# Kernel tuning notes

Measured on AMD Instinct MI355X. Metric: run time of the kernel, lower is better.

Reference implementation:

```python
import jax, jax.numpy as jnp
import numpy as np

SIG_DEPTH = 4  # matches sig_depth init arg


def _outer(a, b):
    # flattened tensor product: [B, m] x [B, n] -> [B, m*n] (row-major, matches signatory layout)
    return (a[:, :, None] * b[:, None, :]).reshape(a.shape[0], -1)


def setup_inputs() -> dict:
    key = jax.random.key(0)
    k1, k2 = jax.random.split(key)
    B, L, Cin = 64, 256, 7
    out_dim = 512
    C = Cin + 1
    sig_channels = sum(C ** k for k in range(1, SIG_DEPTH + 1))  # 4680
    inp = jax.random.normal(k1, (B, L, Cin), dtype=jnp.float32)
    W = jax.random.normal(k2, (out_dim, sig_channels), dtype=jnp.float32) * 0.02
    b = jnp.zeros((out_dim,), dtype=jnp.float32)
    return {"inp": inp, "W": W, "b": b}


def reference(inp, W, b):
    B, L, Cin = inp.shape
    # Augment: prepend time channel linspace(0, 1, L), keep original channels
    t = jnp.broadcast_to(jnp.linspace(0.0, 1.0, L, dtype=inp.dtype)[None, :, None], (B, L, 1))
    x = jnp.concatenate([t, inp], axis=-1)  # [B, L, C]
    C = Cin + 1
    d = SIG_DEPTH
    dx = jnp.transpose(x[:, 1:] - x[:, :-1], (1, 0, 2))  # [L-1, B, C] increments
    init = tuple(jnp.zeros((B, C ** (k + 1)), x.dtype) for k in range(d))  # identity signature (all zero levels)

    def step(levels, v):
        # exp(v) in the truncated tensor algebra: e_k = v^{(x)k} / k!
        e = [v]
        for k in range(1, d):
            e.append(_outer(e[-1], v) / (k + 1))
        # Chen's identity: new_k = a_k + e_k + sum_{i=1}^{k-1} a_i (x) e_{k-i}
        new = []
        for k in range(d):
            acc = levels[k] + e[k]
            for i in range(k):
                acc = acc + _outer(levels[i], e[k - 1 - i])
            new.append(acc)
        sig = jnp.concatenate(new, axis=-1)  # [B, sig_channels]
        return tuple(new), sig

    _, sigs = jax.lax.scan(step, init, dx)  # [L-1, B, sig_channels] (stream=True)
    sigs = jnp.transpose(sigs, (1, 0, 2))   # [B, L-1, sig_channels]
    return sigs @ W.T + b                   # [B, L-1, out_dim]
```

## Files before the change

### kernel.cpp

```cpp
#include <hip/hip_runtime.h>
#include <hip/hip_bf16.h>

#define BATCH 64
#define LSEQ 256
#define CIN 7
#define CC 8
#define NSIG 4680
#define KPAD 4736
#define TSTEPS 255
#define ODIM 512
#define NCHUNK 16
#define CH 16
#define NKT 74
#define BM 256
#define BN 128

typedef __attribute__((ext_vector_type(8))) unsigned short ushort8;
typedef __attribute__((ext_vector_type(8))) __bf16 bf16x8;
typedef __attribute__((ext_vector_type(4))) float f32x4;

__device__ __forceinline__ unsigned short f2bf(float x) {
    __hip_bfloat16 h = __float2bfloat16(x);
    return *(unsigned short*)&h;
}

#define GLDS16(gp, lp)                                                      \
    __builtin_amdgcn_global_load_lds(                                       \
        (const __attribute__((address_space(1))) void*)(gp),                \
        (__attribute__((address_space(3))) void*)(lp), 16, 0, 0)

__global__ __launch_bounds__(512) void sig_ckpt_kernel(const float* __restrict__ inp,
                                                       float* __restrict__ ckpt) {
    __shared__ float sDx[TSTEPS * CC];

    const int b   = blockIdx.x;
    const int tid = threadIdx.x;

    const float* ip = inp + (size_t)b * LSEQ * CIN;
    for (int i = tid; i < TSTEPS * CC; i += 512) {
        int t = i >> 3, c = i & 7;
        sDx[i] = (c == 0) ? (1.0f / 255.0f)
                          : ip[(t + 1) * CIN + (c - 1)] - ip[t * CIN + (c - 1)];
    }
    __syncthreads();

    const int i1 = tid >> 6;
    const int i2 = (tid >> 3) & 7;
    const int i3 = tid & 7;

    float a1own = 0.0f, a2own = 0.0f, a3 = 0.0f;
    float a4[8];
#pragma unroll
    for (int e = 0; e < 8; ++e) a4[e] = 0.0f;

    for (int t = 0; t < 240; ++t) {
        const float* v = &sDx[t * CC];
        const float4 vlo = *(const float4*)&v[0];
        const float4 vhi = *(const float4*)&v[4];
        const float va = v[i1], vb = v[i2], vc = v[i3];
        const float e3s = va * vb * vc * (1.0f / 6.0f);
        const float T4 = e3s * 0.25f + a1own * vb * vc * (1.0f / 6.0f)
                       + a2own * vc * 0.5f + a3;
        a4[0] += vlo.x * T4; a4[1] += vlo.y * T4;
        a4[2] += vlo.z * T4; a4[3] += vlo.w * T4;
        a4[4] += vhi.x * T4; a4[5] += vhi.y * T4;
        a4[6] += vhi.z * T4; a4[7] += vhi.w * T4;
        a3 += e3s + (a1own * vb * 0.5f + a2own) * vc;
        a2own += vb * (0.5f * va + a1own);
        a1own += va;

        if (((t + 1) & 15) == 0) {
            const int c = ((t + 1) >> 4) - 1;
            float* cp = ckpt + ((size_t)b * 15 + c) * NSIG;
            if ((tid & 63) == 0) cp[i1] = a1own;
            if ((tid & 7) == 0) cp[8 + (tid >> 3)] = a2own;
            cp[72 + tid] = a3;
            float4 q0 = {a4[0], a4[1], a4[2], a4[3]};
            float4 q1 = {a4[4], a4[5], a4[6], a4[7]};
            *(float4*)&cp[584 + tid * 8]     = q0;
            *(float4*)&cp[584 + tid * 8 + 4] = q1;
        }
    }
}

__global__ __launch_bounds__(512) void sig_write_kernel(const float* __restrict__ inp,
                                                        const float* __restrict__ ckpt,
                                                        unsigned short* __restrict__ sig) {
    __shared__ float sDx[CH * CC];

    const int chunk = blockIdx.x;
    const int b     = blockIdx.y;
    const int tid   = threadIdx.x;
    const int t0    = chunk * CH;
    const int t1    = (chunk == NCHUNK - 1) ? TSTEPS : t0 + CH;

    const float* ip = inp + (size_t)b * LSEQ * CIN;
    for (int i = tid; i < (t1 - t0) * CC; i += 512) {
        int t = t0 + (i >> 3), c = i & 7;
        sDx[i] = (c == 0) ? (1.0f / 255.0f)
                          : ip[(t + 1) * CIN + (c - 1)] - ip[t * CIN + (c - 1)];
    }
    __syncthreads();

    const int i1 = tid >> 6;
    const int i2 = (tid >> 3) & 7;
    const int i3 = tid & 7;

    float a1own, a2own, a3;
    float a4[8];
    if (chunk == 0) {
        a1own = a2own = a3 = 0.0f;
#pragma unroll
        for (int e = 0; e < 8; ++e) a4[e] = 0.0f;
    } else {
        const float* cp = ckpt + ((size_t)b * 15 + (chunk - 1)) * NSIG;
        a1own = cp[i1];
        a2own = cp[8 + (tid >> 3)];
        a3    = cp[72 + tid];
        float4 q0 = *(const float4*)&cp[584 + tid * 8];
        float4 q1 = *(const float4*)&cp[584 + tid * 8 + 4];
        a4[0] = q0.x; a4[1] = q0.y; a4[2] = q0.z; a4[3] = q0.w;
        a4[4] = q1.x; a4[5] = q1.y; a4[6] = q1.z; a4[7] = q1.w;
    }

    for (int t = t0; t < t1; ++t) {
        const float* v = &sDx[(t - t0) * CC];
        const float4 vlo = *(const float4*)&v[0];
        const float4 vhi = *(const float4*)&v[4];
        const float va = v[i1], vb = v[i2], vc = v[i3];
        const float e3s = va * vb * vc * (1.0f / 6.0f);
        const float T4 = e3s * 0.25f + a1own * vb * vc * (1.0f / 6.0f)
                       + a2own * vc * 0.5f + a3;
        a4[0] += vlo.x * T4; a4[1] += vlo.y * T4;
        a4[2] += vlo.z * T4; a4[3] += vlo.w * T4;
        a4[4] += vhi.x * T4; a4[5] += vhi.y * T4;
        a4[6] += vhi.z * T4; a4[7] += vhi.w * T4;
        a3 += e3s + (a1own * vb * 0.5f + a2own) * vc;
        a2own += vb * (0.5f * va + a1own);
        a1own += va;

        unsigned short* row = sig + ((size_t)b * TSTEPS + t) * KPAD;
        ushort8 pack;
#pragma unroll
        for (int e = 0; e < 8; ++e) pack[e] = f2bf(a4[e]);
        *(ushort8*)(row + 584 + tid * 8) = pack;
        row[72 + tid] = f2bf(a3);
        if ((tid & 63) == 0) row[i1] = f2bf(a1own);
        if ((tid & 7) == 0) row[8 + (tid >> 3)] = f2bf(a2own);
        if (tid >= 448 && tid < 504) row[4232 + tid] = 0;
    }
}

__global__ __launch_bounds__(256) void wcvt_kernel(const float* __restrict__ W,
                                                   unsigned short* __restrict__ Wb) {
    int idx = blockIdx.x * 256 + threadIdx.x;
    if (idx >= ODIM * KPAD) return;
    int n = idx / KPAD, k = idx - n * KPAD;
    Wb[idx] = (k < NSIG) ? f2bf(W[(size_t)n * NSIG + k]) : (unsigned short)0;
}

__global__ __launch_bounds__(512) void gemm_kernel(const unsigned short* __restrict__ A,
                                                   const unsigned short* __restrict__ Wb,
                                                   const float* __restrict__ bias,
                                                   float* __restrict__ out,
                                                   int Mrows) {
    __shared__ unsigned short As[3][BM * 64];
    __shared__ unsigned short Bs[3][BN * 64];

    const int tid = threadIdx.x;
    int nt, mt;
    if (gridDim.y == 64) {
        const int li = blockIdx.y * 4 + blockIdx.x;
        const int x  = li & 7;
        const int j  = li >> 3;
        mt = x * 8 + (j >> 2);
        nt = j & 3;
    } else {
        nt = blockIdx.x; mt = blockIdx.y;
    }
    const int lane = tid & 63;
    const int wv   = tid >> 6;
    const int wr   = wv >> 1;
    const int wc   = wv & 1;
    const int lr   = lane & 15;
    const int lq   = lane >> 4;
    const int sb   = lr & 7;

    const f32x4 z4 = {0.0f, 0.0f, 0.0f, 0.0f};
    f32x4 acc[4][4];
#pragma unroll
    for (int i = 0; i < 4; ++i)
#pragma unroll
        for (int j = 0; j < 4; ++j) acc[i][j] = z4;

    const int srow = tid >> 3;
    const int gcb  = (tid & 7) ^ (srow & 7);
    const int scol = gcb * 8;

    const unsigned short* aptr[4];
    const unsigned short* bptr[2];
#pragma unroll
    for (int i = 0; i < 4; ++i) {
        int gr = mt * BM + i * 64 + srow;
        if (gr >= Mrows) gr = 0;
        aptr[i] = A + (size_t)gr * KPAD + scol;
    }
#pragma unroll
    for (int i = 0; i < 2; ++i)
        bptr[i] = Wb + (size_t)(nt * BN + i * 64 + srow) * KPAD + scol;

    const int kel0 = ((lq)     ^ sb) * 8;
    const int kel1 = ((4 + lq) ^ sb) * 8;

    const int aoff = (wr * 64 + lr) * 64;
    const int boff = (wc * 64 + lr) * 64;

#define STAGE_ALL(buf, koff)                                                \
    do {                                                                    \
        _Pragma("unroll")                                                   \
        for (int i_ = 0; i_ < 4; ++i_)                                      \
            GLDS16(aptr[i_] + (koff),                                       \
                   ((char*)As[buf]) + i_ * 8192 + tid * 16);                \
        _Pragma("unroll")                                                   \
        for (int i_ = 0; i_ < 2; ++i_)                                      \
            GLDS16(bptr[i_] + (koff),                                       \
                   ((char*)Bs[buf]) + i_ * 8192 + tid * 16);                \
    } while (0)

    STAGE_ALL(0, 0);
    STAGE_ALL(1, 64);
    asm volatile("s_waitcnt vmcnt(6)" ::: "memory");
    __builtin_amdgcn_sched_barrier(0);
    __builtin_amdgcn_s_barrier();
    __builtin_amdgcn_sched_barrier(0);

    bf16x8 afP[4], bfP[4], afN[4], bfN[4];
    {
        const unsigned short* as0 = &As[0][0];
        const unsigned short* bs0 = &Bs[0][0];
#pragma unroll
        for (int i = 0; i < 4; ++i)
            afP[i] = *(const bf16x8*)&as0[aoff + i * 1024 + kel0];
#pragma unroll
        for (int j = 0; j < 4; ++j)
            bfP[j] = *(const bf16x8*)&bs0[boff + j * 1024 + kel0];
    }
    __builtin_amdgcn_sched_barrier(0);

    int cur = 0, nxt = 1, nn = 2;
    for (int t = 0; t < NKT; ++t) {
        const unsigned short* as = &As[0][0] + cur * (BM * 64);
        const unsigned short* bs = &Bs[0][0] + cur * (BN * 64);

#pragma unroll
        for (int i = 0; i < 4; ++i)
            afN[i] = *(const bf16x8*)&as[aoff + i * 1024 + kel1];
#pragma unroll
        for (int j = 0; j < 4; ++j)
            bfN[j] = *(const bf16x8*)&bs[boff + j * 1024 + kel1];
        if (t + 2 < NKT) STAGE_ALL(nn, (t + 2) * 64);
        __builtin_amdgcn_sched_barrier(0);

        asm volatile("s_waitcnt lgkmcnt(8)" ::: "memory");
        __builtin_amdgcn_sched_barrier(0);
        __builtin_amdgcn_s_setprio(1);
#pragma unroll
        for (int i = 0; i < 4; ++i)
#pragma unroll
            for (int j = 0; j < 4; ++j)
                acc[i][j] = __builtin_amdgcn_mfma_f32_16x16x32_bf16(
                    afP[i], bfP[j], acc[i][j], 0, 0, 0);
        __builtin_amdgcn_s_setprio(0);
        __builtin_amdgcn_sched_barrier(0);

        asm volatile("s_waitcnt lgkmcnt(0)" ::: "memory");
        __builtin_amdgcn_sched_barrier(0);
        if (t + 1 < NKT) {
            if (t + 2 < NKT) {
                asm volatile("s_waitcnt vmcnt(6)" ::: "memory");
            } else {
                asm volatile("s_waitcnt vmcnt(0)" ::: "memory");
            }
            __builtin_amdgcn_sched_barrier(0);
            __builtin_amdgcn_s_barrier();
            __builtin_amdgcn_sched_barrier(0);
            const unsigned short* asn = &As[0][0] + nxt * (BM * 64);
            const unsigned short* bsn = &Bs[0][0] + nxt * (BN * 64);
#pragma unroll
            for (int i = 0; i < 4; ++i)
                afP[i] = *(const bf16x8*)&asn[aoff + i * 1024 + kel0];
#pragma unroll
            for (int j = 0; j < 4; ++j)
                bfP[j] = *(const bf16x8*)&bsn[boff + j * 1024 + kel0];
            __builtin_amdgcn_sched_barrier(0);
        }

        __builtin_amdgcn_s_setprio(1);
#pragma unroll
        for (int i = 0; i < 4; ++i)
#pragma unroll
            for (int j = 0; j < 4; ++j)
                acc[i][j] = __builtin_amdgcn_mfma_f32_16x16x32_bf16(
                    afN[i], bfN[j], acc[i][j], 0, 0, 0);
        __builtin_amdgcn_s_setprio(0);
        __builtin_amdgcn_sched_barrier(0);

        const int tmp = cur; cur = nxt; nxt = nn; nn = tmp;
    }

    float bn[4];
#pragma unroll
    for (int j = 0; j < 4; ++j)
        bn[j] = bias[nt * BN + wc * 64 + j * 16 + lr];

#pragma unroll
    for (int i = 0; i < 4; ++i) {
        const int mbase = mt * BM + wr * 64 + i * 16 + lq * 4;
#pragma unroll
        for (int r = 0; r < 4; ++r) {
            const int m = mbase + r;
            if (m < Mrows) {
#pragma unroll
                for (int j = 0; j < 4; ++j) {
                    const int n = nt * BN + wc * 64 + j * 16 + lr;
                    out[(size_t)m * ODIM + n] = acc[i][j][r] + bn[j];
                }
            }
        }
    }
#undef STAGE_ALL
}

extern "C" void kernel_launch(void* const* d_in, const int* in_sizes, int n_in,
                              void* d_out, int out_size, void* d_ws, size_t ws_size,
                              hipStream_t stream) {
    const float* inp  = (const float*)d_in[0];
    const float* W    = (const float*)d_in[1];
    const float* bias = (const float*)d_in[2];
    float* out = (float*)d_out;

    const size_t wbBytes = (size_t)ODIM * KPAD * sizeof(unsigned short);
    const size_t sigPB   = (size_t)TSTEPS * KPAD * sizeof(unsigned short);
    const size_t ckptPB  = (size_t)15 * NSIG * sizeof(float);
    const size_t perB    = sigPB + ckptPB;

    int nbMax = (int)((ws_size - wbBytes) / perB);
    if (nbMax > BATCH) nbMax = BATCH;
    if (nbMax < 1) nbMax = 1;

    unsigned short* sig  = (unsigned short*)d_ws;
    float*          ckpt = (float*)((char*)d_ws + (size_t)nbMax * sigPB);
    unsigned short* Wb   = (unsigned short*)((char*)d_ws + (ws_size - wbBytes));

    wcvt_kernel<<<(ODIM * KPAD + 255) / 256, 256, 0, stream>>>(W, Wb);

    for (int b0 = 0; b0 < BATCH; b0 += nbMax) {
        const int nb = (b0 + nbMax <= BATCH) ? nbMax : (BATCH - b0);
        const int Mrows = nb * TSTEPS;
        const float* ipb = inp + (size_t)b0 * LSEQ * CIN;
        sig_ckpt_kernel<<<nb, 512, 0, stream>>>(ipb, ckpt);
        sig_write_kernel<<<dim3(NCHUNK, nb), 512, 0, stream>>>(ipb, ckpt, sig);
        gemm_kernel<<<dim3(ODIM / BN, (Mrows + BM - 1) / BM), 512, 0, stream>>>(
            sig, Wb, bias, out + (size_t)b0 * TSTEPS * ODIM, Mrows);
    }
}
```

Measured before the change: 148.5 us.

## Fuse weight conversion into checkpoint kernel and split checkpoint work per batch

```diff
diff --git a/kernel.cpp b/kernel.cpp
--- a/kernel.cpp
+++ b/kernel.cpp
@@ -14,6 +14,7 @@
 #define NKT 74
 #define BM 256
 #define BN 128
+#define WCVT_BLK 592
 
 typedef __attribute__((ext_vector_type(8))) unsigned short ushort8;
 typedef __attribute__((ext_vector_type(8))) __bf16 bf16x8;
@@ -29,56 +30,74 @@
         (const __attribute__((address_space(1))) void*)(gp),                \
         (__attribute__((address_space(3))) void*)(lp), 16, 0, 0)
 
-__global__ __launch_bounds__(512) void sig_ckpt_kernel(const float* __restrict__ inp,
-                                                       float* __restrict__ ckpt) {
+__global__ __launch_bounds__(512) void prep_kernel(const float* __restrict__ inp,
+                                                   float* __restrict__ ckpt,
+                                                   const float* __restrict__ W,
+                                                   unsigned short* __restrict__ Wb,
+                                                   int nb) {
     __shared__ float sDx[TSTEPS * CC];
-
-    const int b   = blockIdx.x;
+    const int bx  = blockIdx.x;
     const int tid = threadIdx.x;
 
-    const float* ip = inp + (size_t)b * LSEQ * CIN;
-    for (int i = tid; i < TSTEPS * CC; i += 512) {
-        int t = i >> 3, c = i & 7;
-        sDx[i] = (c == 0) ? (1.0f / 255.0f)
-                          : ip[(t + 1) * CIN + (c - 1)] - ip[t * CIN + (c - 1)];
-    }
-    __syncthreads();
-
-    const int i1 = tid >> 6;
-    const int i2 = (tid >> 3) & 7;
-    const int i3 = tid & 7;
-
-    float a1own = 0.0f, a2own = 0.0f, a3 = 0.0f;
-    float a4[8];
-#pragma unroll
-    for (int e = 0; e < 8; ++e) a4[e] = 0.0f;
-
-    for (int t = 0; t < 240; ++t) {
-        const float* v = &sDx[t * CC];
-        const float4 vlo = *(const float4*)&v[0];
-        const float4 vhi = *(const float4*)&v[4];
-        const float va = v[i1], vb = v[i2], vc = v[i3];
-        const float e3s = va * vb * vc * (1.0f / 6.0f);
-        const float T4 = e3s * 0.25f + a1own * vb * vc * (1.0f / 6.0f)
-                       + a2own * vc * 0.5f + a3;
-        a4[0] += vlo.x * T4; a4[1] += vlo.y * T4;
-        a4[2] += vlo.z * T4; a4[3] += vlo.w * T4;
-        a4[4] += vhi.x * T4; a4[5] += vhi.y * T4;
-        a4[6] += vhi.z * T4; a4[7] += vhi.w * T4;
-        a3 += e3s + (a1own * vb * 0.5f + a2own) * vc;
-        a2own += vb * (0.5f * va + a1own);
-        a1own += va;
-
-        if (((t + 1) & 15) == 0) {
-            const int c = ((t + 1) >> 4) - 1;
-            float* cp = ckpt + ((size_t)b * 15 + c) * NSIG;
-            if ((tid & 63) == 0) cp[i1] = a1own;
-            if ((tid & 7) == 0) cp[8 + (tid >> 3)] = a2own;
-            cp[72 + tid] = a3;
-            float4 q0 = {a4[0], a4[1], a4[2], a4[3]};
-            float4 q1 = {a4[4], a4[5], a4[6], a4[7]};
-            *(float4*)&cp[584 + tid * 8]     = q0;
-            *(float4*)&cp[584 + tid * 8 + 4] = q1;
+    if (bx < 4 * nb) {
+        const int b = bx >> 2, q = bx & 3;
+        const float* ip = inp + (size_t)b * LSEQ * CIN;
+        for (int i = tid; i < TSTEPS * CC; i += 512) {
+            int t = i >> 3, c = i & 7;
+            sDx[i] = (c == 0) ? (1.0f / 255.0f)
+                              : ip[(t + 1) * CIN + (c - 1)] - ip[t * CIN + (c - 1)];
+        }
+        __syncthreads();
+
+        const int o  = q * 128 + (tid >> 2);
+        const int e2 = tid & 3;
+        const int i1 = o >> 6, i2 = (o >> 3) & 7, i3 = o & 7;
+        float a1 = 0.0f, a2 = 0.0f, a3 = 0.0f, a4a = 0.0f, a4b = 0.0f;
+
+        for (int t = 0; t < 240; ++t) {
+            const float* v = &sDx[t * CC];
+            const float va = v[i1], vb = v[i2], vc = v[i3];
+            const float vA = v[e2], vB = v[e2 + 4];
+            const float e3s = va * vb * vc * (1.0f / 6.0f);
+            const float T4 = e3s * 0.25f + a1 * vb * vc * (1.0f / 6.0f)
+                           + a2 * vc * 0.5f + a3;
+            a4a += vA * T4;
+            a4b += vB * T4;
+            a3 += e3s + (a1 * vb * 0.5f + a2) * vc;
+            a2 += vb * (0.5f * va + a1);
+            a1 += va;
+
+            if (((t + 1) & 15) == 0) {
+                const int c = ((t + 1) >> 4) - 1;
+                float* cp = ckpt + ((size_t)b * 15 + c) * NSIG;
+                cp[584 + o * 8 + e2]     = a4a;
+                cp[584 + o * 8 + e2 + 4] = a4b;
+                if (e2 == 0) {
+                    cp[72 + o] = a3;
+                    if ((o & 7) == 0)  cp[8 + (o >> 3)] = a2;
+                    if ((o & 63) == 0) cp[i1] = a1;
+                }
+            }
+        }
+    } else {
+        const int vid = (bx - 4 * nb) * 512 + tid;
+        if (vid < ODIM * (KPAD / 8)) {
+            const int n = vid / (KPAD / 8);
+            const int g = vid - n * (KPAD / 8);
+            ushort8 pk;
+            if (g < NSIG / 8) {
+                const float* wp = W + (size_t)n * NSIG + g * 8;
+                float4 f0 = *(const float4*)wp;
+                float4 f1 = *(const float4*)(wp + 4);
+                pk[0] = f2bf(f0.x); pk[1] = f2bf(f0.y);
+                pk[2] = f2bf(f0.z); pk[3] = f2bf(f0.w);
+                pk[4] = f2bf(f1.x); pk[5] = f2bf(f1.y);
+                pk[6] = f2bf(f1.z); pk[7] = f2bf(f1.w);
+            } else {
+#pragma unroll
+                for (int e = 0; e < 8; ++e) pk[e] = 0;
+            }
+            *(ushort8*)(Wb + (size_t)n * KPAD + g * 8) = pk;
         }
     }
 }
@@ -151,14 +170,6 @@
     }
 }
 
-__global__ __launch_bounds__(256) void wcvt_kernel(const float* __restrict__ W,
-                                                   unsigned short* __restrict__ Wb) {
-    int idx = blockIdx.x * 256 + threadIdx.x;
-    if (idx >= ODIM * KPAD) return;
-    int n = idx / KPAD, k = idx - n * KPAD;
-    Wb[idx] = (k < NSIG) ? f2bf(W[(size_t)n * NSIG + k]) : (unsigned short)0;
-}
-
 __global__ __launch_bounds__(512) void gemm_kernel(const unsigned short* __restrict__ A,
                                                    const unsigned short* __restrict__ Wb,
                                                    const float* __restrict__ bias,
@@ -211,7 +222,6 @@
 
     const int kel0 = ((lq)     ^ sb) * 8;
     const int kel1 = ((4 + lq) ^ sb) * 8;
-
     const int aoff = (wr * 64 + lr) * 64;
     const int boff = (wc * 64 + lr) * 64;
 
@@ -352,13 +362,11 @@
     float*          ckpt = (float*)((char*)d_ws + (size_t)nbMax * sigPB);
     unsigned short* Wb   = (unsigned short*)((char*)d_ws + (ws_size - wbBytes));
 
-    wcvt_kernel<<<(ODIM * KPAD + 255) / 256, 256, 0, stream>>>(W, Wb);
-
     for (int b0 = 0; b0 < BATCH; b0 += nbMax) {
         const int nb = (b0 + nbMax <= BATCH) ? nbMax : (BATCH - b0);
         const int Mrows = nb * TSTEPS;
         const float* ipb = inp + (size_t)b0 * LSEQ * CIN;
-        sig_ckpt_kernel<<<nb, 512, 0, stream>>>(ipb, ckpt);
+        prep_kernel<<<4 * nb + WCVT_BLK, 512, 0, stream>>>(ipb, ckpt, W, Wb, nb);
         sig_write_kernel<<<dim3(NCHUNK, nb), 512, 0, stream>>>(ipb, ckpt, sig);
         gemm_kernel<<<dim3(ODIM / BN, (Mrows + BM - 1) / BM), 512, 0, stream>>>(
             sig, Wb, bias, out + (size_t)b0 * TSTEPS * ODIM, Mrows);
```

New measurement: 146.2 us (median of 2 runs). No clear change (-1.5%).
